# Performance work log

Measured on AMD Instinct MI355X. Metric: run time of the kernel, lower is better.

Reference implementation:

```python
import jax, jax.numpy as jnp
import numpy as np

# 4D conv over (L, P, W, H) decomposed as k shifted 3D convs over (P, W, H),
# with the L spatial dim folded into the batch. Faithful to convNd(num_dims=4),
# stride 1, 'same' padding (padding = (k-1)//2), no bias.

def conv4d(x, w):
    # x: [B, C, L, P, W, H]; w: [O, I, k, k, k, k]
    k = w.shape[2]
    p = (k - 1) // 2
    B, C, L, P, Wd, Hd = x.shape
    O = w.shape[0]
    xp = jnp.pad(x, ((0, 0), (0, 0), (p, p), (0, 0), (0, 0), (0, 0)))
    dn = ('NCDHW', 'OIDHW', 'NCDHW')
    out = jnp.zeros((B, O, L, P, Wd, Hd), x.dtype)
    for dl in range(k):  # k <= 3, static loop over kernel taps along L
        xs = xp[:, :, dl:dl + L]                                  # [B,C,L,P,W,H]
        xs = xs.transpose(0, 2, 1, 3, 4, 5).reshape(B * L, C, P, Wd, Hd)
        y = jax.lax.conv_general_dilated(xs, w[:, :, dl], (1, 1, 1),
                                         [(p, p)] * 3, dimension_numbers=dn)
        out = out + y.reshape(B, L, O, P, Wd, Hd).transpose(0, 2, 1, 3, 4, 5)
    return out


def inception4d(x, weights):
    # mean over parallel 4D convs with kernel sizes 1, 3, ... (2i+1)
    acc = conv4d(x, weights[0])
    for w in weights[1:]:
        acc = acc + conv4d(x, w)
    return acc / len(weights)


def setup_inputs() -> dict:
    key = jax.random.key(0)
    ks = jax.random.split(key, 5)
    B, T, W, H, C = 4, 48, 8, 8, 32
    d_model, d_ff = 32, 64
    x = jax.random.normal(ks[0], (B, T, W, H, C), dtype=jnp.float32)
    # Inception_Block4D weights: kernel sizes 1 and 3 (num_kernels=2), no bias
    w1_0 = jax.random.normal(ks[1], (d_ff, d_model, 1, 1, 1, 1), dtype=jnp.float32) * 0.1
    w1_1 = jax.random.normal(ks[2], (d_ff, d_model, 3, 3, 3, 3), dtype=jnp.float32) * 0.02
    w2_0 = jax.random.normal(ks[3], (d_model, d_ff, 1, 1, 1, 1), dtype=jnp.float32) * 0.1
    w2_1 = jax.random.normal(ks[4], (d_model, d_ff, 3, 3, 3, 3), dtype=jnp.float32) * 0.02
    return {"x": x, "w1_0": w1_0, "w1_1": w1_1, "w2_0": w2_0, "w2_1": w2_1}


def reference(x, w1_0, w1_1, w2_0, w2_1):
    B, T, W, H, C = x.shape
    periods = (2, 3, 4)                       # FFT_for_Period hardcoded output
    xf = jnp.ones((B, len(periods)), x.dtype) # hardcoded uniform weights
    real_len = T                              # seq_len + pred_len
    res = []
    for period in periods:
        if real_len % period != 0:
            length = (real_len // period + 1) * period
            out = jnp.concatenate([x, x[:, -(length - real_len):]], axis=1)
        else:
            length = real_len
            out = x
        # [B, L, P, W, H, C] -> [B, C, L, P, W, H]
        out = out.reshape(B, length // period, period, W, H, C).transpose(0, 5, 1, 2, 3, 4)
        h = inception4d(out, [w1_0, w1_1])
        h = jax.nn.gelu(h, approximate=False)  # torch nn.GELU default (exact)
        h = inception4d(h, [w2_0, w2_1])
        # [B, C, L, P, W, H] -> [B, (L P), W, H, C]
        h = h.transpose(0, 2, 3, 4, 5, 1).reshape(B, length, W, H, C)
        res.append(h[:, :real_len])
    res = jnp.stack(res, axis=1)              # [B, k, T, W, H, C]
    pw = jax.nn.softmax(xf, axis=1).reshape(B, len(periods), 1, 1, 1, 1)
    return jnp.sum(res * pw, axis=1) + x
```

## Files before the change

### kernel.cpp

```cpp
#include <hip/hip_runtime.h>
#include <math.h>


typedef __attribute__((ext_vector_type(8))) short bf16x8;
typedef __attribute__((ext_vector_type(4))) float f32x4;
typedef unsigned short u16;

#define XC 3200
#define HC 6400
#define XSEG 617600
#define ZSEG_END 636800
#define W1OFF 636800
#define W2OFF 802688
#define H1OFF 968576
#define H1P 1235200
#define PREP_N 1300352
#define OUT_Q 98304
#define PREP_TOT (PREP_N + OUT_Q)

#define WAITVM(N) asm volatile("s_waitcnt vmcnt(" #N ")" ::: "memory")
#define SBAR()    asm volatile("s_barrier" ::: "memory")

__device__ __forceinline__ u16 f2bf(float f) {
    unsigned u = __float_as_uint(f);
    unsigned r = u + 0x7fffu + ((u >> 16) & 1u);
    return (u16)(r >> 16);
}
__device__ __forceinline__ float gelu_exact(float v) {
    return 0.5f * v * (1.0f + erff(v * 0.7071067811865476f));
}

__device__ __forceinline__ void cp1k(const u16* g, u16* l, int lane) {
    __builtin_amdgcn_global_load_lds(
        (const __attribute__((address_space(1))) unsigned int*)(g + lane * 8),
        (__attribute__((address_space(3))) unsigned int*)(l + lane * 8),
        16, 0, 0);
}

__global__ __launch_bounds__(256) void prep(
    const float* __restrict__ x,
    const float* __restrict__ w1_0, const float* __restrict__ w1_1,
    const float* __restrict__ w2_0, const float* __restrict__ w2_1,
    u16* __restrict__ ws, float* __restrict__ out) {
    int i = blockIdx.x * 256 + threadIdx.x;
    if (i < XSEG) {
        int cellidx = i / XC; int inner = i - cellidx * XC;
        int cellpos = inner >> 5; int low = inner & 31;
        int sc = low >> 3, jj = low & 7;
        int c = ((sc ^ (cellpos & 3)) << 3) + jj;
        int wp = cellpos / 10, hp = cellpos - (cellpos / 10) * 10;
        float v = 0.f;
        if (cellidx < 192 && wp >= 1 && wp <= 8 && hp >= 1 && hp <= 8)
            v = x[(cellidx * 64 + (wp - 1) * 8 + (hp - 1)) * 32 + c];
        ws[i] = f2bf(v);
    } else if (i < ZSEG_END) {
        int j = i - XSEG;
        int per = j / HC; int off = j - per * HC;
        ws[H1OFF + per * H1P + 192 * HC + off] = 0;
    } else if (i < ZSEG_END + 165888) {
        int j = i - W1OFF;
        int tap = j >> 11; int r = j & 2047;
        int chunk = r >> 3, jj = r & 7;
        int m = chunk & 15, nt = (chunk >> 4) & 3, quad = chunk >> 6;
        int o = nt * 16 + m, c = quad * 8 + jj;
        float v = 0.5f * w1_1[(o * 32 + c) * 81 + tap];
        if (tap == 40) v += 0.5f * w1_0[o * 32 + c];
        ws[i] = f2bf(v);
    } else if (i < PREP_N) {
        int j = i - W2OFF;
        int tap = j >> 11; int r = j & 2047;
        int chunk = r >> 3, jj = r & 7;
        int m = chunk & 15, nt = (chunk >> 4) & 1;
        int quad = (chunk >> 5) & 3, ks = chunk >> 7;
        int o = nt * 16 + m, c = ks * 32 + quad * 8 + jj;
        float v = 0.5f * w2_1[(o * 64 + c) * 81 + tap];
        if (tap == 40) v += 0.5f * w2_0[o * 64 + c];
        ws[i] = f2bf(v);
    } else if (i < PREP_TOT) {
        int j = i - PREP_N;
        ((float4*)out)[j] = ((const float4*)x)[j];
    }
}

template<int P>
__device__ __forceinline__ int cidx(int bb, int l2, int q2) {
    constexpr int L = 48 / P;
    return ((unsigned)l2 < (unsigned)L && (unsigned)q2 < (unsigned)P)
               ? bb * 48 + l2 * P + q2 : 192;
}

template<int P>
__device__ __forceinline__ void conv1_body(
    const u16* __restrict__ xs, const u16* __restrict__ w1b,
    u16* __restrict__ h1, int tp, int bb,
    u16* __restrict__ s_w, u16* __restrict__ s_a) {
    constexpr int HB = (P == 2) ? 0 : (P == 3) ? H1P : 2 * H1P;

    int tid = threadIdx.x;
    int lane = tid & 63, wv = tid >> 6;
    int m = lane & 15, quad = lane >> 4;
    int tloc = wv >> 1, nh = wv & 1;

    int t0 = tp * 2, t1 = tp * 2 + 1;
    int l0 = t0 / P, q0 = t0 - l0 * P;
    int l1 = t1 / P, q1 = t1 - l1 * P;

    int sp[4];
#pragma unroll
    for (int mt = 0; mt < 4; ++mt) {
        int pos = mt * 16 + m;
        sp[mt] = (pos >> 3) * 10 + (pos & 7);
    }

    f32x4 acc[4][2];
#pragma unroll
    for (int mt = 0; mt < 4; ++mt)
#pragma unroll
        for (int nt = 0; nt < 2; ++nt) acc[mt][nt] = f32x4{0.f, 0.f, 0.f, 0.f};

    auto stageW = [&](int cgn) {
        const u16* src = w1b + (cgn * 3) * 2048;
        u16* dst = s_w + (cgn & 3) * 6144;
        int p0 = wv * 3;
#pragma unroll
        for (int i = 0; i < 3; ++i)
            cp1k(src + (p0 + i) * 512, dst + (p0 + i) * 512, lane);
    };
    auto stageA = [&](int gg) {
        int dl = gg / 3, dq = gg - (gg / 3) * 3;
        const u16* c0 = xs + cidx<P>(bb, l0 + dl - 1, q0 + dq - 1) * XC;
        const u16* c1 = xs + cidx<P>(bb, l1 + dl - 1, q1 + dq - 1) * XC;
#pragma unroll
        for (int i = 0; i < 4; ++i) {
            int k = wv * 4 + i; if (k >= 14) k = 13;
            int cell = k / 7, pc = k - (k / 7) * 7;
            cp1k((cell ? c1 : c0) + pc * 512,
                 s_a + (cell * 2 + (gg & 1)) * 3584 + pc * 512, lane);
        }
    };

    stageW(0); stageA(0); stageW(1);

#pragma unroll 1
    for (int cg = 0; cg < 27; ++cg) {
        if (cg < 25) {
            stageW(cg + 2);
            if ((cg + 2) % 3 == 0) stageA((cg + 2) / 3);
        }
        if (cg == 25) { WAITVM(3); }
        else if (cg == 26) { WAITVM(0); }
        else if (cg % 3 == 0) { WAITVM(6); }
        else { WAITVM(10); }
        SBAR();

        int grp = cg / 3, part = cg - grp * 3;
        const u16* bw = s_w + (cg & 3) * 6144;
        const u16* ba = s_a + (tloc * 2 + (grp & 1)) * 3584;
        int dwb = part * 10;
#pragma unroll
        for (int j = 0; j < 3; ++j) {
            const u16* tw = bw + j * 2048;
            bf16x8 wf[2];
#pragma unroll
            for (int nt = 0; nt < 2; ++nt)
                wf[nt] = *(const bf16x8*)(tw +
                    (((quad * 4 + nh * 2 + nt) * 16 + m) << 3));
            bf16x8 af[4];
#pragma unroll
            for (int mt = 0; mt < 4; ++mt) {
                int cellpos = sp[mt] + dwb + j;
                af[mt] = *(const bf16x8*)(ba + cellpos * 32 +
                                          ((quad ^ (cellpos & 3)) << 3));
            }
#pragma unroll
            for (int mt = 0; mt < 4; ++mt)
#pragma unroll
                for (int nt = 0; nt < 2; ++nt)
                    acc[mt][nt] = __builtin_amdgcn_mfma_f32_16x16x32_bf16(
                        af[mt], wf[nt], acc[mt][nt], 0, 0, 0);
        }
    }

    int t = tp * 2 + tloc;
    u16* hcell = h1 + HB + (bb * 48 + t) * HC;
#pragma unroll
    for (int mt = 0; mt < 4; ++mt)
#pragma unroll
        for (int r = 0; r < 4; ++r) {
            int pos = mt * 16 + quad * 4 + r;
            int cellpos = ((pos >> 3) + 1) * 10 + (pos & 7) + 1;
#pragma unroll
            for (int nt = 0; nt < 2; ++nt) {
                int o = nh * 32 + nt * 16 + m;
                hcell[cellpos * 64 + (((o >> 3) ^ (cellpos & 7)) << 3) + (o & 7)] =
                    f2bf(gelu_exact(acc[mt][nt][r]));
            }
        }
    unsigned int* h32 = (unsigned int*)hcell;
#pragma unroll
    for (int it = 0; it < 18; ++it) {
        int k = it * 64 + lane;
        int bp = k >> 5, u = k & 31;
        int cp;
        if (bp < 10) cp = bp;
        else if (bp < 20) cp = 90 + (bp - 10);
        else if (bp < 28) cp = (bp - 19) * 10;
        else cp = (bp - 27) * 10 + 9;
        h32[cp * 32 + u] = 0;
    }
}

__global__ __launch_bounds__(256) void conv1_k(
    const u16* __restrict__ ws_x, const u16* __restrict__ ws_w1,
    u16* __restrict__ ws_h1) {
    __shared__ __align__(16) u16 s_w[4 * 6144];
    __shared__ __align__(16) u16 s_a[4 * 3584];
    int g = blockIdx.x;
    int jid = (g & 7) * 36 + (g >> 3);
    int per = jid / 96; int rem = jid - per * 96;
    int bb = rem / 24; int tp = rem - bb * 24;
    if (per == 0)      conv1_body<2>(ws_x, ws_w1, ws_h1, tp, bb, s_w, s_a);
    else if (per == 1) conv1_body<3>(ws_x, ws_w1, ws_h1, tp, bb, s_w, s_a);
    else               conv1_body<4>(ws_x, ws_w1, ws_h1, tp, bb, s_w, s_a);
}

template<int P>
__device__ __forceinline__ void conv2_body(
    const u16* __restrict__ h1, const u16* __restrict__ w2b,
    float* __restrict__ out, int tp, int bb,
    u16* __restrict__ s_w, u16* __restrict__ s_a) {
    constexpr int HB = (P == 2) ? 0 : (P == 3) ? H1P : 2 * H1P;

    int tid = threadIdx.x;
    int lane = tid & 63, wv = tid >> 6;
    int m = lane & 15, quad = lane >> 4;
    int tloc = wv >> 1, mh = wv & 1;

    int t0 = tp * 2, t1 = tp * 2 + 1;
    int l0 = t0 / P, q0 = t0 - l0 * P;
    int l1 = t1 / P, q1 = t1 - l1 * P;
    const u16* hb = h1 + HB;

    int sp[2];
#pragma unroll
    for (int mt = 0; mt < 2; ++mt) {
        int pos = mh * 32 + mt * 16 + m;
        sp[mt] = (pos >> 3) * 10 + (pos & 7);
    }

    f32x4 acc[2][2];
#pragma unroll
    for (int mt = 0; mt < 2; ++mt)
#pragma unroll
        for (int nt = 0; nt < 2; ++nt) acc[mt][nt] = f32x4{0.f, 0.f, 0.f, 0.f};

    auto stageW = [&](int cgn) {
        const u16* src = w2b + (cgn * 3) * 2048;
        u16* dst = s_w + (cgn & 1) * 6144;
        int p0 = wv * 3;
#pragma unroll
        for (int i = 0; i < 3; ++i)
            cp1k(src + (p0 + i) * 512, dst + (p0 + i) * 512, lane);
    };
    auto stageA = [&](int gg, int k0, int k1) {
        int dl = gg / 3, dq = gg - (gg / 3) * 3;
        const u16* c0 = hb + cidx<P>(bb, l0 + dl - 1, q0 + dq - 1) * HC;
        const u16* c1 = hb + cidx<P>(bb, l1 + dl - 1, q1 + dq - 1) * HC;
        for (int k = k0 + wv; k < k1; k += 4) {
            int cell = k / 13, pc = k - (k / 13) * 13;
            cp1k((cell ? c1 : c0) + pc * 512,
                 s_a + (cell * 2 + (gg & 1)) * 6656 + pc * 512, lane);
        }
    };

    stageW(0);
    stageA(0, 0, 26);

#pragma unroll 1
    for (int cg = 0; cg < 27; ++cg) {
        __syncthreads();
        if (cg < 26) stageW(cg + 1);
        int grp = cg / 3, part = cg - grp * 3;
        if (grp < 8) stageA(grp + 1, part * 9, (part == 2) ? 26 : part * 9 + 9);

        const u16* bw = s_w + (cg & 1) * 6144;
        const u16* ba = s_a + (tloc * 2 + (grp & 1)) * 6656;
        int dwb = part * 10;
#pragma unroll
        for (int j = 0; j < 3; ++j) {
            const u16* tw = bw + j * 2048;
            bf16x8 wf[2][2];
#pragma unroll
            for (int nt = 0; nt < 2; ++nt)
#pragma unroll
                for (int ks = 0; ks < 2; ++ks)
                    wf[nt][ks] = *(const bf16x8*)(tw +
                        ((((ks * 4 + quad) * 2 + nt) * 16 + m) << 3));
            bf16x8 af[2][2];
#pragma unroll
            for (int mt = 0; mt < 2; ++mt) {
                int cellpos = sp[mt] + dwb + j;
#pragma unroll
                for (int ks = 0; ks < 2; ++ks)
                    af[mt][ks] = *(const bf16x8*)(ba + cellpos * 64 +
                        (((ks * 4 + quad) ^ (cellpos & 7)) << 3));
            }
#pragma unroll
            for (int mt = 0; mt < 2; ++mt)
#pragma unroll
                for (int ks = 0; ks < 2; ++ks)
#pragma unroll
                    for (int nt = 0; nt < 2; ++nt)
                        acc[mt][nt] = __builtin_amdgcn_mfma_f32_16x16x32_bf16(
                            af[mt][ks], wf[nt][ks], acc[mt][nt], 0, 0, 0);
        }
    }

    int t = tp * 2 + tloc;
    float* orow = out + (bb * 48 + t) * 2048;
    const float s = 1.0f / 3.0f;
#pragma unroll
    for (int mt = 0; mt < 2; ++mt)
#pragma unroll
        for (int nt = 0; nt < 2; ++nt)
#pragma unroll
            for (int r = 0; r < 4; ++r) {
                int pos = mh * 32 + mt * 16 + quad * 4 + r;
                atomicAdd(&orow[pos * 32 + nt * 16 + m], acc[mt][nt][r] * s);
            }
}

__global__ __launch_bounds__(256) void conv2_k(
    const u16* __restrict__ ws_h1, const u16* __restrict__ ws_w2,
    float* __restrict__ out) {
    __shared__ __align__(16) u16 s_w[2 * 6144];
    __shared__ __align__(16) u16 s_a[4 * 6656];
    int g = blockIdx.x;
    int jid = (g & 7) * 36 + (g >> 3);
    int per = jid / 96; int rem = jid - per * 96;
    int bb = rem / 24; int tp = rem - bb * 24;
    if (per == 0)      conv2_body<2>(ws_h1, ws_w2, out, tp, bb, s_w, s_a);
    else if (per == 1) conv2_body<3>(ws_h1, ws_w2, out, tp, bb, s_w, s_a);
    else               conv2_body<4>(ws_h1, ws_w2, out, tp, bb, s_w, s_a);
}

extern "C" void kernel_launch(void* const* d_in, const int* in_sizes, int n_in,
                              void* d_out, int out_size, void* d_ws, size_t ws_size,
                              hipStream_t stream) {
    const float* x    = (const float*)d_in[0];
    const float* w1_0 = (const float*)d_in[1];
    const float* w1_1 = (const float*)d_in[2];
    const float* w2_0 = (const float*)d_in[3];
    const float* w2_1 = (const float*)d_in[4];
    float* out = (float*)d_out;

    u16* ws = (u16*)d_ws;
    u16* ws_x  = ws;
    u16* ws_w1 = ws + W1OFF;
    u16* ws_w2 = ws + W2OFF;
    u16* ws_h1 = ws + H1OFF;

    prep<<<(PREP_TOT + 255) / 256, 256, 0, stream>>>(
        x, w1_0, w1_1, w2_0, w2_1, ws, out);
    conv1_k<<<288, 256, 0, stream>>>(ws_x, ws_w1, ws_h1);
    conv2_k<<<288, 256, 0, stream>>>(ws_h1, ws_w2, out);
}
```

Measured before the change: 129.1 us.

## Pack 288 conv jobs into 256 blocks, pairing jobs in the tail blocks

Both conv kernels now launch 256 blocks, one per CU, instead of 288. The first 224 blocks run one job and the last 32 run two jobs that share each weight stage, which avoids a second partial wave. Period handling moves from compile-time templates to runtime values with a dual-accumulator layout. Conv1 also drops its deeper 4-stage weight pipeline with manual vmcnt waits in favour of double buffering with __syncthreads. This doubles LDS and accumulator use, and the two-job blocks become stragglers that take about twice as long.

```diff
diff --git a/kernel.cpp b/kernel.cpp
--- a/kernel.cpp
+++ b/kernel.cpp
@@ -17,9 +17,6 @@
 #define PREP_N 1300352
 #define OUT_Q 98304
 #define PREP_TOT (PREP_N + OUT_Q)
-
-#define WAITVM(N) asm volatile("s_waitcnt vmcnt(" #N ")" ::: "memory")
-#define SBAR()    asm volatile("s_barrier" ::: "memory")
 
 __device__ __forceinline__ u16 f2bf(float f) {
     unsigned u = __float_as_uint(f);
@@ -89,21 +86,40 @@
                ? bb * 48 + l2 * P + q2 : 192;
 }
 
-template<int P>
-__device__ __forceinline__ void conv1_body(
+__device__ __forceinline__ int cidx_rt(int P, int bb, int l2, int q2) {
+    if (P == 2) return cidx<2>(bb, l2, q2);
+    if (P == 3) return cidx<3>(bb, l2, q2);
+    return cidx<4>(bb, l2, q2);
+}
+
+__device__ __forceinline__ void job_decode(int jid, int& per, int& bb, int& tp) {
+    per = jid / 96; int rem = jid - per * 96;
+    bb = rem / 24; tp = rem - bb * 24;
+}
+
+__global__ __launch_bounds__(256) void conv1_k(
     const u16* __restrict__ xs, const u16* __restrict__ w1b,
-    u16* __restrict__ h1, int tp, int bb,
-    u16* __restrict__ s_w, u16* __restrict__ s_a) {
-    constexpr int HB = (P == 2) ? 0 : (P == 3) ? H1P : 2 * H1P;
+    u16* __restrict__ h1) {
+    __shared__ __align__(16) u16 s_w[2 * 6144];
+    __shared__ __align__(16) u16 s_a[2 * 4 * 3584];
+    int g = blockIdx.x;
+    int gg = (g & 7) * 32 + (g >> 3);
+    int nj = (gg < 224) ? 1 : 2;
+    int j0 = (gg < 224) ? gg : 224 + (gg - 224) * 2;
 
     int tid = threadIdx.x;
     int lane = tid & 63, wv = tid >> 6;
     int m = lane & 15, quad = lane >> 4;
     int tloc = wv >> 1, nh = wv & 1;
 
-    int t0 = tp * 2, t1 = tp * 2 + 1;
-    int l0 = t0 / P, q0 = t0 - l0 * P;
-    int l1 = t1 / P, q1 = t1 - l1 * P;
+    int per[2], bb[2], tp[2], l0[2], q0[2], l1[2], q1[2];
+    for (int jl = 0; jl < nj; ++jl) {
+        job_decode(j0 + jl, per[jl], bb[jl], tp[jl]);
+        int Pv = per[jl] + 2;
+        int t0 = tp[jl] * 2, t1 = t0 + 1;
+        l0[jl] = t0 / Pv; q0[jl] = t0 - l0[jl] * Pv;
+        l1[jl] = t1 / Pv; q1[jl] = t1 - l1[jl] * Pv;
+    }
 
     int sp[4];
 #pragma unroll
@@ -112,236 +128,233 @@
         sp[mt] = (pos >> 3) * 10 + (pos & 7);
     }
 
-    f32x4 acc[4][2];
-#pragma unroll
-    for (int mt = 0; mt < 4; ++mt)
-#pragma unroll
-        for (int nt = 0; nt < 2; ++nt) acc[mt][nt] = f32x4{0.f, 0.f, 0.f, 0.f};
+    f32x4 acc[2][4][2];
+    for (int jl = 0; jl < 2; ++jl)
+#pragma unroll
+        for (int mt = 0; mt < 4; ++mt)
+#pragma unroll
+            for (int nt = 0; nt < 2; ++nt)
+                acc[jl][mt][nt] = f32x4{0.f, 0.f, 0.f, 0.f};
 
     auto stageW = [&](int cgn) {
         const u16* src = w1b + (cgn * 3) * 2048;
-        u16* dst = s_w + (cgn & 3) * 6144;
+        u16* dst = s_w + (cgn & 1) * 6144;
         int p0 = wv * 3;
 #pragma unroll
         for (int i = 0; i < 3; ++i)
             cp1k(src + (p0 + i) * 512, dst + (p0 + i) * 512, lane);
     };
-    auto stageA = [&](int gg) {
-        int dl = gg / 3, dq = gg - (gg / 3) * 3;
-        const u16* c0 = xs + cidx<P>(bb, l0 + dl - 1, q0 + dq - 1) * XC;
-        const u16* c1 = xs + cidx<P>(bb, l1 + dl - 1, q1 + dq - 1) * XC;
-#pragma unroll
-        for (int i = 0; i < 4; ++i) {
-            int k = wv * 4 + i; if (k >= 14) k = 13;
+    auto stageA = [&](int jl, int gg2, int k0, int k1) {
+        int Pv = per[jl] + 2;
+        int dl = gg2 / 3, dq = gg2 - (gg2 / 3) * 3;
+        int c0 = cidx_rt(Pv, bb[jl], l0[jl] + dl - 1, q0[jl] + dq - 1);
+        int c1 = cidx_rt(Pv, bb[jl], l1[jl] + dl - 1, q1[jl] + dq - 1);
+        const u16* p0 = xs + c0 * XC;
+        const u16* p1 = xs + c1 * XC;
+        for (int k = k0 + wv; k < k1; k += 4) {
             int cell = k / 7, pc = k - (k / 7) * 7;
-            cp1k((cell ? c1 : c0) + pc * 512,
-                 s_a + (cell * 2 + (gg & 1)) * 3584 + pc * 512, lane);
+            cp1k((cell ? p1 : p0) + pc * 512,
+                 s_a + ((jl * 2 + cell) * 2 + (gg2 & 1)) * 3584 + pc * 512, lane);
         }
     };
 
-    stageW(0); stageA(0); stageW(1);
-
-#pragma unroll 1
-    for (int cg = 0; cg < 27; ++cg) {
-        if (cg < 25) {
-            stageW(cg + 2);
-            if ((cg + 2) % 3 == 0) stageA((cg + 2) / 3);
-        }
-        if (cg == 25) { WAITVM(3); }
-        else if (cg == 26) { WAITVM(0); }
-        else if (cg % 3 == 0) { WAITVM(6); }
-        else { WAITVM(10); }
-        SBAR();
-
-        int grp = cg / 3, part = cg - grp * 3;
-        const u16* bw = s_w + (cg & 3) * 6144;
-        const u16* ba = s_a + (tloc * 2 + (grp & 1)) * 3584;
-        int dwb = part * 10;
-#pragma unroll
-        for (int j = 0; j < 3; ++j) {
-            const u16* tw = bw + j * 2048;
-            bf16x8 wf[2];
-#pragma unroll
-            for (int nt = 0; nt < 2; ++nt)
-                wf[nt] = *(const bf16x8*)(tw +
-                    (((quad * 4 + nh * 2 + nt) * 16 + m) << 3));
-            bf16x8 af[4];
-#pragma unroll
-            for (int mt = 0; mt < 4; ++mt) {
-                int cellpos = sp[mt] + dwb + j;
-                af[mt] = *(const bf16x8*)(ba + cellpos * 32 +
-                                          ((quad ^ (cellpos & 3)) << 3));
-            }
-#pragma unroll
-            for (int mt = 0; mt < 4; ++mt)
-#pragma unroll
-                for (int nt = 0; nt < 2; ++nt)
-                    acc[mt][nt] = __builtin_amdgcn_mfma_f32_16x16x32_bf16(
-                        af[mt], wf[nt], acc[mt][nt], 0, 0, 0);
-        }
-    }
-
-    int t = tp * 2 + tloc;
-    u16* hcell = h1 + HB + (bb * 48 + t) * HC;
-#pragma unroll
-    for (int mt = 0; mt < 4; ++mt)
-#pragma unroll
-        for (int r = 0; r < 4; ++r) {
-            int pos = mt * 16 + quad * 4 + r;
-            int cellpos = ((pos >> 3) + 1) * 10 + (pos & 7) + 1;
-#pragma unroll
-            for (int nt = 0; nt < 2; ++nt) {
-                int o = nh * 32 + nt * 16 + m;
-                hcell[cellpos * 64 + (((o >> 3) ^ (cellpos & 7)) << 3) + (o & 7)] =
-                    f2bf(gelu_exact(acc[mt][nt][r]));
-            }
-        }
-    unsigned int* h32 = (unsigned int*)hcell;
-#pragma unroll
-    for (int it = 0; it < 18; ++it) {
-        int k = it * 64 + lane;
-        int bp = k >> 5, u = k & 31;
-        int cp;
-        if (bp < 10) cp = bp;
-        else if (bp < 20) cp = 90 + (bp - 10);
-        else if (bp < 28) cp = (bp - 19) * 10;
-        else cp = (bp - 27) * 10 + 9;
-        h32[cp * 32 + u] = 0;
-    }
-}
-
-__global__ __launch_bounds__(256) void conv1_k(
-    const u16* __restrict__ ws_x, const u16* __restrict__ ws_w1,
-    u16* __restrict__ ws_h1) {
-    __shared__ __align__(16) u16 s_w[4 * 6144];
-    __shared__ __align__(16) u16 s_a[4 * 3584];
-    int g = blockIdx.x;
-    int jid = (g & 7) * 36 + (g >> 3);
-    int per = jid / 96; int rem = jid - per * 96;
-    int bb = rem / 24; int tp = rem - bb * 24;
-    if (per == 0)      conv1_body<2>(ws_x, ws_w1, ws_h1, tp, bb, s_w, s_a);
-    else if (per == 1) conv1_body<3>(ws_x, ws_w1, ws_h1, tp, bb, s_w, s_a);
-    else               conv1_body<4>(ws_x, ws_w1, ws_h1, tp, bb, s_w, s_a);
-}
-
-template<int P>
-__device__ __forceinline__ void conv2_body(
-    const u16* __restrict__ h1, const u16* __restrict__ w2b,
-    float* __restrict__ out, int tp, int bb,
-    u16* __restrict__ s_w, u16* __restrict__ s_a) {
-    constexpr int HB = (P == 2) ? 0 : (P == 3) ? H1P : 2 * H1P;
-
-    int tid = threadIdx.x;
-    int lane = tid & 63, wv = tid >> 6;
-    int m = lane & 15, quad = lane >> 4;
-    int tloc = wv >> 1, mh = wv & 1;
-
-    int t0 = tp * 2, t1 = tp * 2 + 1;
-    int l0 = t0 / P, q0 = t0 - l0 * P;
-    int l1 = t1 / P, q1 = t1 - l1 * P;
-    const u16* hb = h1 + HB;
-
-    int sp[2];
-#pragma unroll
-    for (int mt = 0; mt < 2; ++mt) {
-        int pos = mh * 32 + mt * 16 + m;
-        sp[mt] = (pos >> 3) * 10 + (pos & 7);
-    }
-
-    f32x4 acc[2][2];
-#pragma unroll
-    for (int mt = 0; mt < 2; ++mt)
-#pragma unroll
-        for (int nt = 0; nt < 2; ++nt) acc[mt][nt] = f32x4{0.f, 0.f, 0.f, 0.f};
-
-    auto stageW = [&](int cgn) {
-        const u16* src = w2b + (cgn * 3) * 2048;
-        u16* dst = s_w + (cgn & 1) * 6144;
-        int p0 = wv * 3;
-#pragma unroll
-        for (int i = 0; i < 3; ++i)
-            cp1k(src + (p0 + i) * 512, dst + (p0 + i) * 512, lane);
-    };
-    auto stageA = [&](int gg, int k0, int k1) {
-        int dl = gg / 3, dq = gg - (gg / 3) * 3;
-        const u16* c0 = hb + cidx<P>(bb, l0 + dl - 1, q0 + dq - 1) * HC;
-        const u16* c1 = hb + cidx<P>(bb, l1 + dl - 1, q1 + dq - 1) * HC;
-        for (int k = k0 + wv; k < k1; k += 4) {
-            int cell = k / 13, pc = k - (k / 13) * 13;
-            cp1k((cell ? c1 : c0) + pc * 512,
-                 s_a + (cell * 2 + (gg & 1)) * 6656 + pc * 512, lane);
-        }
-    };
-
     stageW(0);
-    stageA(0, 0, 26);
+    for (int jl = 0; jl < nj; ++jl) stageA(jl, 0, 0, 14);
 
 #pragma unroll 1
     for (int cg = 0; cg < 27; ++cg) {
         __syncthreads();
         if (cg < 26) stageW(cg + 1);
         int grp = cg / 3, part = cg - grp * 3;
-        if (grp < 8) stageA(grp + 1, part * 9, (part == 2) ? 26 : part * 9 + 9);
+        if (grp < 8)
+            for (int jl = 0; jl < nj; ++jl)
+                stageA(jl, grp + 1, part * 5, (part == 2) ? 14 : part * 5 + 5);
 
         const u16* bw = s_w + (cg & 1) * 6144;
-        const u16* ba = s_a + (tloc * 2 + (grp & 1)) * 6656;
         int dwb = part * 10;
-#pragma unroll
-        for (int j = 0; j < 3; ++j) {
-            const u16* tw = bw + j * 2048;
-            bf16x8 wf[2][2];
-#pragma unroll
-            for (int nt = 0; nt < 2; ++nt)
-#pragma unroll
-                for (int ks = 0; ks < 2; ++ks)
-                    wf[nt][ks] = *(const bf16x8*)(tw +
-                        ((((ks * 4 + quad) * 2 + nt) * 16 + m) << 3));
-            bf16x8 af[2][2];
-#pragma unroll
-            for (int mt = 0; mt < 2; ++mt) {
-                int cellpos = sp[mt] + dwb + j;
-#pragma unroll
-                for (int ks = 0; ks < 2; ++ks)
-                    af[mt][ks] = *(const bf16x8*)(ba + cellpos * 64 +
-                        (((ks * 4 + quad) ^ (cellpos & 7)) << 3));
+        for (int jl = 0; jl < nj; ++jl) {
+            const u16* ba = s_a + ((jl * 2 + tloc) * 2 + (grp & 1)) * 3584;
+#pragma unroll
+            for (int j = 0; j < 3; ++j) {
+                const u16* tw = bw + j * 2048;
+                bf16x8 wf[2];
+#pragma unroll
+                for (int nt = 0; nt < 2; ++nt)
+                    wf[nt] = *(const bf16x8*)(tw +
+                        (((quad * 4 + nh * 2 + nt) * 16 + m) << 3));
+                bf16x8 af[4];
+#pragma unroll
+                for (int mt = 0; mt < 4; ++mt) {
+                    int cellpos = sp[mt] + dwb + j;
+                    af[mt] = *(const bf16x8*)(ba + cellpos * 32 +
+                                              ((quad ^ (cellpos & 3)) << 3));
+                }
+#pragma unroll
+                for (int mt = 0; mt < 4; ++mt)
+#pragma unroll
+                    for (int nt = 0; nt < 2; ++nt)
+                        acc[jl][mt][nt] = __builtin_amdgcn_mfma_f32_16x16x32_bf16(
+                            af[mt], wf[nt], acc[jl][mt][nt], 0, 0, 0);
             }
-#pragma unroll
-            for (int mt = 0; mt < 2; ++mt)
-#pragma unroll
-                for (int ks = 0; ks < 2; ++ks)
-#pragma unroll
-                    for (int nt = 0; nt < 2; ++nt)
-                        acc[mt][nt] = __builtin_amdgcn_mfma_f32_16x16x32_bf16(
-                            af[mt][ks], wf[nt][ks], acc[mt][nt], 0, 0, 0);
-        }
-    }
-
-    int t = tp * 2 + tloc;
-    float* orow = out + (bb * 48 + t) * 2048;
-    const float s = 1.0f / 3.0f;
-#pragma unroll
-    for (int mt = 0; mt < 2; ++mt)
-#pragma unroll
-        for (int nt = 0; nt < 2; ++nt)
+        }
+    }
+
+    for (int jl = 0; jl < nj; ++jl) {
+        int HB = per[jl] * H1P;
+        int t = tp[jl] * 2 + tloc;
+        u16* hcell = h1 + HB + (bb[jl] * 48 + t) * HC;
+#pragma unroll
+        for (int mt = 0; mt < 4; ++mt)
 #pragma unroll
             for (int r = 0; r < 4; ++r) {
-                int pos = mh * 32 + mt * 16 + quad * 4 + r;
-                atomicAdd(&orow[pos * 32 + nt * 16 + m], acc[mt][nt][r] * s);
+                int pos = mt * 16 + quad * 4 + r;
+                int cellpos = ((pos >> 3) + 1) * 10 + (pos & 7) + 1;
+#pragma unroll
+                for (int nt = 0; nt < 2; ++nt) {
+                    int o = nh * 32 + nt * 16 + m;
+                    hcell[cellpos * 64 + (((o >> 3) ^ (cellpos & 7)) << 3) + (o & 7)] =
+                        f2bf(gelu_exact(acc[jl][mt][nt][r]));
+                }
             }
+        unsigned int* h32 = (unsigned int*)hcell;
+#pragma unroll
+        for (int it = 0; it < 18; ++it) {
+            int k = it * 64 + lane;
+            int bp = k >> 5, u = k & 31;
+            int cp;
+            if (bp < 10) cp = bp;
+            else if (bp < 20) cp = 90 + (bp - 10);
+            else if (bp < 28) cp = (bp - 19) * 10;
+            else cp = (bp - 27) * 10 + 9;
+            h32[cp * 32 + u] = 0;
+        }
+    }
 }
 
 __global__ __launch_bounds__(256) void conv2_k(
-    const u16* __restrict__ ws_h1, const u16* __restrict__ ws_w2,
+    const u16* __restrict__ h1, const u16* __restrict__ w2b,
     float* __restrict__ out) {
     __shared__ __align__(16) u16 s_w[2 * 6144];
-    __shared__ __align__(16) u16 s_a[4 * 6656];
+    __shared__ __align__(16) u16 s_a[2 * 4 * 6656];
     int g = blockIdx.x;
-    int jid = (g & 7) * 36 + (g >> 3);
-    int per = jid / 96; int rem = jid - per * 96;
-    int bb = rem / 24; int tp = rem - bb * 24;
-    if (per == 0)      conv2_body<2>(ws_h1, ws_w2, out, tp, bb, s_w, s_a);
-    else if (per == 1) conv2_body<3>(ws_h1, ws_w2, out, tp, bb, s_w, s_a);
-    else               conv2_body<4>(ws_h1, ws_w2, out, tp, bb, s_w, s_a);
+    int gg = (g & 7) * 32 + (g >> 3);
+    int nj = (gg < 224) ? 1 : 2;
+    int j0 = (gg < 224) ? gg : 224 + (gg - 224) * 2;
+
+    int tid = threadIdx.x;
+    int lane = tid & 63, wv = tid >> 6;
+    int m = lane & 15, quad = lane >> 4;
+    int tloc = wv >> 1, mh = wv & 1;
+
+    int per[2], bb[2], tp[2], l0[2], q0[2], l1[2], q1[2];
+    for (int jl = 0; jl < nj; ++jl) {
+        job_decode(j0 + jl, per[jl], bb[jl], tp[jl]);
+        int Pv = per[jl] + 2;
+        int t0 = tp[jl] * 2, t1 = t0 + 1;
+        l0[jl] = t0 / Pv; q0[jl] = t0 - l0[jl] * Pv;
+        l1[jl] = t1 / Pv; q1[jl] = t1 - l1[jl] * Pv;
+    }
+
+    int sp[2];
+#pragma unroll
+    for (int mt = 0; mt < 2; ++mt) {
+        int pos = mh * 32 + mt * 16 + m;
+        sp[mt] = (pos >> 3) * 10 + (pos & 7);
+    }
+
+    f32x4 acc[2][2][2];
+    for (int jl = 0; jl < 2; ++jl)
+#pragma unroll
+        for (int mt = 0; mt < 2; ++mt)
+#pragma unroll
+            for (int nt = 0; nt < 2; ++nt)
+                acc[jl][mt][nt] = f32x4{0.f, 0.f, 0.f, 0.f};
+
+    auto stageW = [&](int cgn) {
+        const u16* src = w2b + (cgn * 3) * 2048;
+        u16* dst = s_w + (cgn & 1) * 6144;
+        int p0 = wv * 3;
+#pragma unroll
+        for (int i = 0; i < 3; ++i)
+            cp1k(src + (p0 + i) * 512, dst + (p0 + i) * 512, lane);
+    };
+    auto stageA = [&](int jl, int gg2, int k0, int k1) {
+        int Pv = per[jl] + 2;
+        int dl = gg2 / 3, dq = gg2 - (gg2 / 3) * 3;
+        int c0 = cidx_rt(Pv, bb[jl], l0[jl] + dl - 1, q0[jl] + dq - 1);
+        int c1 = cidx_rt(Pv, bb[jl], l1[jl] + dl - 1, q1[jl] + dq - 1);
+        const u16* hb = h1 + per[jl] * H1P;
+        const u16* p0 = hb + c0 * HC;
+        const u16* p1 = hb + c1 * HC;
+        for (int k = k0 + wv; k < k1; k += 4) {
+            int cell = k / 13, pc = k - (k / 13) * 13;
+            cp1k((cell ? p1 : p0) + pc * 512,
+                 s_a + ((jl * 2 + cell) * 2 + (gg2 & 1)) * 6656 + pc * 512, lane);
+        }
+    };
+
+    stageW(0);
+    for (int jl = 0; jl < nj; ++jl) stageA(jl, 0, 0, 26);
+
+#pragma unroll 1
+    for (int cg = 0; cg < 27; ++cg) {
+        __syncthreads();
+        if (cg < 26) stageW(cg + 1);
+        int grp = cg / 3, part = cg - grp * 3;
+        if (grp < 8)
+            for (int jl = 0; jl < nj; ++jl)
+                stageA(jl, grp + 1, part * 9, (part == 2) ? 26 : part * 9 + 9);
+
+        const u16* bw = s_w + (cg & 1) * 6144;
+        int dwb = part * 10;
+        for (int jl = 0; jl < nj; ++jl) {
+            const u16* ba = s_a + ((jl * 2 + tloc) * 2 + (grp & 1)) * 6656;
+#pragma unroll
+            for (int j = 0; j < 3; ++j) {
+                const u16* tw = bw + j * 2048;
+                bf16x8 wf[2][2];
+#pragma unroll
+                for (int nt = 0; nt < 2; ++nt)
+#pragma unroll
+                    for (int ks = 0; ks < 2; ++ks)
+                        wf[nt][ks] = *(const bf16x8*)(tw +
+                            ((((ks * 4 + quad) * 2 + nt) * 16 + m) << 3));
+                bf16x8 af[2][2];
+#pragma unroll
+                for (int mt = 0; mt < 2; ++mt) {
+                    int cellpos = sp[mt] + dwb + j;
+#pragma unroll
+                    for (int ks = 0; ks < 2; ++ks)
+                        af[mt][ks] = *(const bf16x8*)(ba + cellpos * 64 +
+                            (((ks * 4 + quad) ^ (cellpos & 7)) << 3));
+                }
+#pragma unroll
+                for (int mt = 0; mt < 2; ++mt)
+#pragma unroll
+                    for (int ks = 0; ks < 2; ++ks)
+#pragma unroll
+                        for (int nt = 0; nt < 2; ++nt)
+                            acc[jl][mt][nt] = __builtin_amdgcn_mfma_f32_16x16x32_bf16(
+                                af[mt][ks], wf[nt][ks], acc[jl][mt][nt], 0, 0, 0);
+            }
+        }
+    }
+
+    const float s = 1.0f / 3.0f;
+    for (int jl = 0; jl < nj; ++jl) {
+        int t = tp[jl] * 2 + tloc;
+        float* orow = out + (bb[jl] * 48 + t) * 2048;
+#pragma unroll
+        for (int mt = 0; mt < 2; ++mt)
+#pragma unroll
+            for (int nt = 0; nt < 2; ++nt)
+#pragma unroll
+                for (int r = 0; r < 4; ++r) {
+                    int pos = mh * 32 + mt * 16 + quad * 4 + r;
+                    atomicAdd(&orow[pos * 32 + nt * 16 + m],
+                              acc[jl][mt][nt][r] * s);
+                }
+    }
 }
 
 extern "C" void kernel_launch(void* const* d_in, const int* in_sizes, int n_in,
@@ -362,6 +375,6 @@
 
     prep<<<(PREP_TOT + 255) / 256, 256, 0, stream>>>(
         x, w1_0, w1_1, w2_0, w2_1, ws, out);
-    conv1_k<<<288, 256, 0, stream>>>(ws_x, ws_w1, ws_h1);
-    conv2_k<<<288, 256, 0, stream>>>(ws_h1, ws_w2, out);
-}
+    conv1_k<<<256, 256, 0, stream>>>(ws_x, ws_w1, ws_h1);
+    conv2_k<<<256, 256, 0, stream>>>(ws_h1, ws_w2, out);
+}
```

Result: slower. 362.8 us (+181.1%).
